# Optimization experiments

Measured on AMD Instinct MI355X. Metric: run time of the kernel, lower is better.

Reference implementation:

```python
import jax, jax.numpy as jnp
import numpy as np
from jax import lax

jax.config.update("jax_enable_x64", True)  # source casts distances to double for sinkhorn

N_E = 512
E_DIM = 256
NUM_EXPERTS = 10
B = 8192
MU = 0.25
BETA = 1.0
SK_EPS = 0.01
SK_ITERS = 100


def setup_inputs() -> dict:
    key = jax.random.key(0)
    k0, k1, k2, k3 = jax.random.split(key, 4)
    x = jax.random.normal(k0, (B, E_DIM), dtype=jnp.float32)
    label = jax.random.randint(k1, (N_E,), 0, 10)  # cluster id per code of codebook 0
    gate_probs = jax.random.uniform(k2, (B, NUM_EXPERTS), dtype=jnp.float32)
    # embeddings initialized uniform(-1/n_e, 1/n_e) as in __init__
    emb = jax.random.uniform(k3, (NUM_EXPERTS + 1, N_E, E_DIM), dtype=jnp.float32,
                             minval=-1.0 / N_E, maxval=1.0 / N_E)
    return {"x": x, "label": label, "idx": 0, "gate_probs": gate_probs, "emb": emb}


def _sinkhorn(d, eps, iters):
    # standard SwAV-style sinkhorn (as used in UniTok/LETTER); d: [B, K] float64
    logits = -d / eps
    Q = jnp.exp(logits - jnp.max(logits))  # max-shift is a no-op after global normalization
    Q = (Q / jnp.sum(Q)).T  # [K, B]
    K, Bn = Q.shape

    def step(Q, _):
        Q = Q / (jnp.sum(Q, axis=1, keepdims=True) * K)
        Q = Q / (jnp.sum(Q, axis=0, keepdims=True) * Bn)
        return Q, None

    Q, _ = lax.scan(step, Q, None, length=iters)
    return (Q * Bn).T  # [B, K]


def _assign(latent, W):
    d = (jnp.sum(latent ** 2, axis=1, keepdims=True)
         + jnp.sum(W ** 2, axis=1)[None, :]
         - 2.0 * latent @ W.T)  # [B, n_e]
    mx, mn = jnp.max(d), jnp.min(d)
    mid = (mx + mn) / 2
    amp = mx - mid + 1e-5
    d = ((d - mid) / amp).astype(jnp.float64)
    Q = _sinkhorn(d, SK_EPS, SK_ITERS)
    return jnp.argmax(Q, axis=-1)  # [B]


def reference(x, label, idx, gate_probs, emb):
    latent = x.reshape(-1, E_DIM)  # [B, D]
    nb = latent.shape[0]

    # per-expert sinkhorn assignment (use_sk=True, sk_epsilon>0 path)
    indices_all = jax.vmap(lambda W: _assign(latent, W))(emb)          # [11, B]
    xq_all = jax.vmap(lambda W, i: W[i])(emb, indices_all)              # [11, B, D]

    x_q = jnp.einsum('be,ebd->bd', gate_probs, xq_all[:NUM_EXPERTS])
    x_q = 0.95 * x_q + 0.05 * xq_all[NUM_EXPERTS]

    # diversity loss on codebook 0: positive = another code in the same cluster
    ind0 = indices_all[0]                      # [B]
    clusters = label[ind0]                     # [B]
    ar = jnp.arange(N_E)
    pos_mask = (label[None, :] == clusters[:, None]) & (ar[None, :] != ind0[:, None])
    y_true = jnp.argmax(pos_mask, axis=1)      # deterministic positive sample
    sim = x_q @ emb[0].T                       # [B, n_e]
    sim = sim.at[jnp.arange(nb), ind0].add(-1e12)  # mask self-similarity
    logp = jax.nn.log_softmax(sim, axis=-1)
    diversity_loss = -jnp.mean(logp[jnp.arange(nb), y_true])

    commitment_loss = jnp.mean((lax.stop_gradient(x_q) - x) ** 2)
    codebook_loss = jnp.mean((x_q - lax.stop_gradient(x)) ** 2)
    loss = codebook_loss + MU * commitment_loss + BETA * diversity_loss

    # selected index per token: codebook of top expert
    expert_id = jnp.argmax(gate_probs, axis=1)          # [B] in [0,10)
    indices = indices_all.T[jnp.arange(nb), expert_id]  # [B]

    x_q_out = x + lax.stop_gradient(x_q - x)  # straight-through
    return x_q_out, loss, indices
```

## Files before the change

### kernel.cpp

```cpp
#include <hip/hip_runtime.h>
#include <cstdint>
#include <cstddef>

#define NTOK 8192
#define NE 512
#define EDIM 256
#define NEXPALL 11
#define NITER 100

static __device__ __forceinline__ double wredsum(double x) {
  for (int o = 32; o > 0; o >>= 1) x += __shfl_down(x, o, 64);
  return x;
}

static constexpr double S32 = 2.3283064365386963e-10;
static constexpr double Q32 = 4294967296.0;

__global__ void k_init(unsigned* colmin, double* r0, double* r1, double* uprev,
                       unsigned* dmaxA, unsigned* dminA, int* conv_iter, double* sums) {
  int i = blockIdx.x * 256 + threadIdx.x;
  if (i < NEXPALL * NTOK) colmin[i] = 0x7F800000u;
  if (i < NEXPALL * NE) { r0[i] = 0.0; r1[i] = 0.0; uprev[i] = 0.0; }
  if (i < NEXPALL) { dmaxA[i] = 0u; dminA[i] = 0x7F800000u; conv_iter[i] = 1 << 30; }
  if (i < 2) sums[i] = 0.0;
}

__global__ __launch_bounds__(256) void k_npsq(const float* __restrict__ p, float* __restrict__ o, int rows) {
  int r = blockIdx.x * 16 + (threadIdx.x >> 4);
  int l = threadIdx.x & 15;
  if (r >= rows) return;
  const float* a = p + (size_t)r * EDIM;
  int leaf = l >> 3;
  int j = l & 7;
  const float* base = a + leaf * 128 + j;
  float acc = __fmul_rn(base[0], base[0]);
#pragma unroll
  for (int i = 8; i < 128; i += 8) {
    float v = base[i];
    acc = __fadd_rn(acc, __fmul_rn(v, v));
  }
  acc = __fadd_rn(acc, __shfl_xor(acc, 1, 64));
  acc = __fadd_rn(acc, __shfl_xor(acc, 2, 64));
  acc = __fadd_rn(acc, __shfl_xor(acc, 4, 64));
  float other = __shfl_xor(acc, 8, 64);
  float tot = (leaf == 0) ? __fadd_rn(acc, other) : __fadd_rn(other, acc);
  if (l == 0) o[r] = tot;
}

__global__ __launch_bounds__(256) void k_gemm_d(const float* __restrict__ x, const float* __restrict__ emb,
                                                const float* __restrict__ sx, const float* __restrict__ sw,
                                                float* __restrict__ bigF,
                                                unsigned* __restrict__ colminA,
                                                unsigned* __restrict__ dmaxA,
                                                unsigned* __restrict__ dminA) {
  int bx = blockIdx.x, by = blockIdx.y, e = blockIdx.z;
  int tid = threadIdx.x;
  int tx = tid & 15, ty = tid >> 4;
  int b0 = bx * 64, k0 = by * 64;

  __shared__ float xs[64][17];
  __shared__ float es[64][17];
  __shared__ float sxs[64];
  __shared__ float sws[64];
  __shared__ unsigned colm[64];
  __shared__ float ttile[64][68];
  __shared__ float wrx[4], wrn[4];

  if (tid < 64) { sxs[tid] = sx[b0 + tid]; colm[tid] = 0x7F800000u; }
  else if (tid < 128) { sws[tid - 64] = sw[e * NE + k0 + tid - 64]; }

  float acc[4][4] = {};
  const float* xbase = x + (size_t)b0 * EDIM;
  const float* wbase = emb + ((size_t)e * NE + k0) * EDIM;
  int lr = tid >> 2;
  int lc = (tid & 3) * 4;

  for (int kc = 0; kc < EDIM; kc += 16) {
    float4 xv = *(const float4*)(xbase + (size_t)lr * EDIM + kc + lc);
    float4 wv = *(const float4*)(wbase + (size_t)lr * EDIM + kc + lc);
    __syncthreads();
    xs[lr][lc + 0] = xv.x; xs[lr][lc + 1] = xv.y; xs[lr][lc + 2] = xv.z; xs[lr][lc + 3] = xv.w;
    es[lr][lc + 0] = wv.x; es[lr][lc + 1] = wv.y; es[lr][lc + 2] = wv.z; es[lr][lc + 3] = wv.w;
    __syncthreads();
#pragma unroll
    for (int kk = 0; kk < 16; ++kk) {
      float a0 = xs[ty][kk], a1 = xs[ty + 16][kk], a2 = xs[ty + 32][kk], a3 = xs[ty + 48][kk];
      float w0 = es[tx][kk], w1 = es[tx + 16][kk], w2 = es[tx + 32][kk], w3 = es[tx + 48][kk];
      acc[0][0] = fmaf(a0, w0, acc[0][0]); acc[0][1] = fmaf(a0, w1, acc[0][1]);
      acc[0][2] = fmaf(a0, w2, acc[0][2]); acc[0][3] = fmaf(a0, w3, acc[0][3]);
      acc[1][0] = fmaf(a1, w0, acc[1][0]); acc[1][1] = fmaf(a1, w1, acc[1][1]);
      acc[1][2] = fmaf(a1, w2, acc[1][2]); acc[1][3] = fmaf(a1, w3, acc[1][3]);
      acc[2][0] = fmaf(a2, w0, acc[2][0]); acc[2][1] = fmaf(a2, w1, acc[2][1]);
      acc[2][2] = fmaf(a2, w2, acc[2][2]); acc[2][3] = fmaf(a2, w3, acc[2][3]);
      acc[3][0] = fmaf(a3, w0, acc[3][0]); acc[3][1] = fmaf(a3, w1, acc[3][1]);
      acc[3][2] = fmaf(a3, w2, acc[3][2]); acc[3][3] = fmaf(a3, w3, acc[3][3]);
    }
  }

  float dmx = -3.0e38f, dmn = 3.0e38f;
#pragma unroll
  for (int i = 0; i < 4; ++i) {
    float cmin = 3.0e38f;
#pragma unroll
    for (int j = 0; j < 4; ++j) {
      float m2 = __fmul_rn(2.0f, acc[i][j]);
      float dv = __fsub_rn(__fadd_rn(sxs[ty + 16 * i], sws[tx + 16 * j]), m2);
      ttile[tx + 16 * j][ty + 16 * i] = dv;
      dmx = fmaxf(dmx, dv); dmn = fminf(dmn, dv);
      cmin = fminf(cmin, dv);
    }
    atomicMin(&colm[ty + 16 * i], __float_as_uint(cmin));
  }
  for (int o = 32; o > 0; o >>= 1) {
    dmx = fmaxf(dmx, __shfl_down(dmx, o, 64));
    dmn = fminf(dmn, __shfl_down(dmn, o, 64));
  }
  int wv = tid >> 6, ln = tid & 63;
  if (ln == 0) { wrx[wv] = dmx; wrn[wv] = dmn; }
  __syncthreads();
  if (tid == 0) {
    float m1 = fmaxf(fmaxf(wrx[0], wrx[1]), fmaxf(wrx[2], wrx[3]));
    float m2 = fminf(fminf(wrn[0], wrn[1]), fminf(wrn[2], wrn[3]));
    atomicMax(dmaxA + e, __float_as_uint(m1));
    atomicMin(dminA + e, __float_as_uint(m2));
  }
  if (tid < 64) atomicMin(colminA + (size_t)e * NTOK + b0 + tid, colm[tid]);
  int orow = tid >> 2, oc = (tid & 3) << 4;
  float* ob = bigF + ((size_t)e * NE + k0 + orow) * NTOK + b0 + oc;
  *(float4*)(ob + 0) = *(float4*)&ttile[orow][oc + 0];
  *(float4*)(ob + 4) = *(float4*)&ttile[orow][oc + 4];
  *(float4*)(ob + 8) = *(float4*)&ttile[orow][oc + 8];
  *(float4*)(ob + 12) = *(float4*)&ttile[orow][oc + 12];
}

__global__ __launch_bounds__(256) void k_prep(const unsigned* __restrict__ colminA,
                                              const unsigned* __restrict__ dmaxA,
                                              const unsigned* __restrict__ dminA,
                                              double* __restrict__ cml, double* __restrict__ v) {
  int e = blockIdx.y;
  int b = blockIdx.x * 256 + threadIdx.x;
  float mx = __uint_as_float(dmaxA[e]);
  float mn = __uint_as_float(dminA[e]);
  float mid = __fmul_rn(__fadd_rn(mx, mn), 0.5f);
  float amp = __fadd_rn(__fsub_rn(mx, mid), 1e-5f);
  float cminf = __uint_as_float(colminA[(size_t)e * NTOK + b]);
  float dn = __fdiv_rn(__fsub_rn(cminf, mid), amp);
  double l = (-(double)dn) / 0.01;
  cml[(size_t)e * NTOK + b] = l;
  v[(size_t)e * NTOK + b] = exp(l);
}

__global__ __launch_bounds__(256) void k_build(float* __restrict__ bigF,
                                               const unsigned* __restrict__ dmaxA,
                                               const unsigned* __restrict__ dminA,
                                               const double* __restrict__ cml, const double* __restrict__ v0,
                                               double* __restrict__ r0) {
  int bx = blockIdx.x, k = blockIdx.y, e = blockIdx.z;
  int tid = threadIdx.x;
  float mx = __uint_as_float(dmaxA[e]);
  float mn = __uint_as_float(dminA[e]);
  float mid = __fmul_rn(__fadd_rn(mx, mn), 0.5f);
  float amp = __fadd_rn(__fsub_rn(mx, mid), 1e-5f);
  size_t rb = ((size_t)e * NE + k) * NTOK;
  int cb = bx * 2048 + tid * 8;
  float4 fa = *(const float4*)(bigF + rb + cb);
  float4 fb = *(const float4*)(bigF + rb + cb + 4);
  float din[8] = {fa.x, fa.y, fa.z, fa.w, fb.x, fb.y, fb.z, fb.w};
  unsigned qo[8];
  double racc = 0.0;
#pragma unroll
  for (int j = 0; j < 8; ++j) {
    int b = cb + j;
    float dn = __fdiv_rn(__fsub_rn(din[j], mid), amp);
    double l = (-(double)dn) / 0.01;
    double t = l - cml[(size_t)e * NTOK + b];
    double Bv = exp(t);
    double qd = (1.0 - Bv) * Q32;
    qd = fmin(fmax(qd, 0.0), 4294967295.0);
    unsigned q = (unsigned)llrint(qd);
    qo[j] = q;
    double Bq = fma(-(double)q, S32, 1.0);
    racc = fma(Bq, v0[(size_t)e * NTOK + b], racc);
  }
  uint4 oa = make_uint4(qo[0], qo[1], qo[2], qo[3]);
  uint4 ob2 = make_uint4(qo[4], qo[5], qo[6], qo[7]);
  *(uint4*)((unsigned*)bigF + rb + cb) = oa;
  *(uint4*)((unsigned*)bigF + rb + cb + 4) = ob2;
  racc = wredsum(racc);
  __shared__ double pr[4];
  int wv = tid >> 6, ln = tid & 63;
  if (ln == 0) pr[wv] = racc;
  __syncthreads();
  if (tid == 0) atomicAdd(&r0[e * NE + k], (pr[0] + pr[1]) + (pr[2] + pr[3]));
}

__global__ __launch_bounds__(256) void k_iter_a(const unsigned* __restrict__ bigU,
                                                const double* __restrict__ rc, double* __restrict__ rn,
                                                double* __restrict__ v, double* __restrict__ uprev,
                                                int* conv_iter, int t) {
  int e = blockIdx.y, bx = blockIdx.x, tid = threadIdx.x;
  int ci = ((volatile int*)conv_iter)[e];
  if (t > ci) {
    if (bx == 0) {
      int k2 = tid * 2;
      rn[e * NE + k2] = rc[e * NE + k2];
      rn[e * NE + k2 + 1] = rc[e * NE + k2 + 1];
    }
    return;
  }
  __shared__ double us[NE];
  __shared__ int okf;
  if (tid == 0) okf = 1;
  int k2 = tid * 2;
  double u0 = 1.0 / (512.0 * rc[e * NE + k2]);
  double u1 = 1.0 / (512.0 * rc[e * NE + k2 + 1]);
  us[k2] = u0; us[k2 + 1] = u1;
  __syncthreads();
  if (bx == 0) {
    double p0 = uprev[e * NE + k2], p1 = uprev[e * NE + k2 + 1];
    bool ok = (fabs(u0 - p0) <= 1e-13 * fabs(u0)) && (fabs(u1 - p1) <= 1e-13 * fabs(u1));
    if (!ok) okf = 0;
    uprev[e * NE + k2] = u0; uprev[e * NE + k2 + 1] = u1;
    rn[e * NE + k2] = 0.0; rn[e * NE + k2 + 1] = 0.0;
  }
  __syncthreads();
  if (bx == 0 && tid == 0 && okf) atomicMin(conv_iter + e, t);

  int col = bx * 256 + tid;
  const unsigned* cp = bigU + (size_t)e * NE * NTOK + col;
  double c0 = 0, c1 = 0, c2 = 0, c3 = 0;
#pragma unroll 2
  for (int k = 0; k < NE; k += 4) {
    unsigned q0 = cp[(size_t)(k + 0) * NTOK];
    unsigned q1 = cp[(size_t)(k + 1) * NTOK];
    unsigned q2 = cp[(size_t)(k + 2) * NTOK];
    unsigned q3 = cp[(size_t)(k + 3) * NTOK];
    c0 = fma(us[k + 0], fma(-(double)q0, S32, 1.0), c0);
    c1 = fma(us[k + 1], fma(-(double)q1, S32, 1.0), c1);
    c2 = fma(us[k + 2], fma(-(double)q2, S32, 1.0), c2);
    c3 = fma(us[k + 3], fma(-(double)q3, S32, 1.0), c3);
  }
  double c = (c0 + c1) + (c2 + c3);
  v[(size_t)e * NTOK + col] = 1.0 / (8192.0 * c);
}

__global__ __launch_bounds__(256) void k_iter_b(const unsigned* __restrict__ bigU,
                                                const double* __restrict__ v, double* __restrict__ rn,
                                                const int* conv_iter, int t) {
  int e = blockIdx.z;
  if (t > ((volatile int*)conv_iter)[e]) return;
  int bx = blockIdx.x, ky = blockIdx.y, tid = threadIdx.x;
  int wv = tid >> 6, ln = tid & 63;
  int cb = bx * 2048 + tid * 8;
  const double* vb = v + (size_t)e * NTOK + cb;
  double v0 = vb[0], v1 = vb[1], v2 = vb[2], v3 = vb[3];
  double v4 = vb[4], v5 = vb[5], v6 = vb[6], v7 = vb[7];
  __shared__ double part[16][4];
  size_t ebase = (size_t)e * NE * NTOK;
  for (int rr = 0; rr < 4; ++rr) {
#pragma unroll 4
    for (int kk = 0; kk < 16; ++kk) {
      int k = ky * 64 + rr * 16 + kk;
      const unsigned* rp = bigU + ebase + (size_t)k * NTOK + cb;
      uint4 qa = *(const uint4*)rp;
      uint4 qb = *(const uint4*)(rp + 4);
      double p;
      p = v0 * fma(-(double)qa.x, S32, 1.0);
      p = fma(v1, fma(-(double)qa.y, S32, 1.0), p);
      p = fma(v2, fma(-(double)qa.z, S32, 1.0), p);
      p = fma(v3, fma(-(double)qa.w, S32, 1.0), p);
      p = fma(v4, fma(-(double)qb.x, S32, 1.0), p);
      p = fma(v5, fma(-(double)qb.y, S32, 1.0), p);
      p = fma(v6, fma(-(double)qb.z, S32, 1.0), p);
      p = fma(v7, fma(-(double)qb.w, S32, 1.0), p);
      p = wredsum(p);
      if (ln == 0) part[kk][wv] = p;
    }
    __syncthreads();
    if (tid < 16)
      atomicAdd(&rn[e * NE + ky * 64 + rr * 16 + tid],
                (part[tid][0] + part[tid][1]) + (part[tid][2] + part[tid][3]));
    __syncthreads();
  }
}

__global__ __launch_bounds__(256) void k_final(const unsigned* __restrict__ bigU,
                                               const double* __restrict__ rfin, int* __restrict__ idxs) {
  int e = blockIdx.y, bx = blockIdx.x, tid = threadIdx.x;
  __shared__ double us[NE];
  int k2 = tid * 2;
  us[k2] = 1.0 / (512.0 * rfin[e * NE + k2]);
  us[k2 + 1] = 1.0 / (512.0 * rfin[e * NE + k2 + 1]);
  __syncthreads();
  int col = bx * 256 + tid;
  const unsigned* cp = bigU + (size_t)e * NE * NTOK + col;
  double best = -1.0;
  int bi = 0;
#pragma unroll 4
  for (int k = 0; k < NE; ++k) {
    double s = us[k] * fma(-(double)cp[(size_t)k * NTOK], S32, 1.0);
    if (s > best) { best = s; bi = k; }
  }
  idxs[(size_t)e * NTOK + col] = bi;
}

__global__ __launch_bounds__(256) void k_mix(const float* __restrict__ x, const float* __restrict__ gate,
                                             const float* __restrict__ emb, const int* __restrict__ idxs,
                                             float* __restrict__ xq, float* __restrict__ out0,
                                             float* __restrict__ outIdx, double* __restrict__ mse_sum) {
  int tid = threadIdx.x;
  int sub = tid >> 5, lane = tid & 31;
  int tok = blockIdx.x * 8 + sub;
  float acc[8] = {0, 0, 0, 0, 0, 0, 0, 0};
#pragma unroll
  for (int ee = 0; ee < 10; ++ee) {
    int id = idxs[(size_t)ee * NTOK + tok];
    float g = gate[tok * 10 + ee];
    const float* er = emb + ((size_t)ee * NE + id) * EDIM + lane;
#pragma unroll
    for (int dd = 0; dd < 8; ++dd) acc[dd] = fmaf(g, er[32 * dd], acc[dd]);
  }
  int id10 = idxs[(size_t)10 * NTOK + tok];
  const float* es = emb + ((size_t)10 * NE + id10) * EDIM + lane;
  double ms = 0.0;
#pragma unroll
  for (int dd = 0; dd < 8; ++dd) {
    int d = lane + 32 * dd;
    float q = 0.95f * acc[dd] + 0.05f * es[32 * dd];
    float xv = x[(size_t)tok * EDIM + d];
    float df = q - xv;
    out0[(size_t)tok * EDIM + d] = xv + df;
    xq[(size_t)tok * EDIM + d] = q;
    ms += (double)df * (double)df;
  }
  ms = wredsum(ms);
  __shared__ double pr[4];
  int wv = tid >> 6, ln = tid & 63;
  if (ln == 0) pr[wv] = ms;
  __syncthreads();
  if (tid == 0) atomicAdd(mse_sum, (pr[0] + pr[1]) + (pr[2] + pr[3]));
  if (lane == 0) {
    const float* gr = gate + tok * 10;
    float bg = gr[0];
    int be = 0;
#pragma unroll
    for (int ee = 1; ee < 10; ++ee) { float g = gr[ee]; if (g > bg) { bg = g; be = ee; } }
    outIdx[tok] = (float)idxs[(size_t)be * NTOK + tok];
  }
}

__global__ __launch_bounds__(256) void k_simgemm(const float* __restrict__ xq, const float* __restrict__ emb,
                                                 float* __restrict__ sim) {
  int bx = blockIdx.x, by = blockIdx.y, tid = threadIdx.x;
  int tx = tid & 15, ty = tid >> 4;
  int b0 = bx * 64, j0 = by * 64;
  __shared__ float xs[64][17];
  __shared__ float es[64][17];
  __shared__ float tt[64][68];
  float acc[4][4] = {};
  int lr = tid >> 2, lc = (tid & 3) * 4;
  for (int kc = 0; kc < EDIM; kc += 16) {
    float4 xv = *(const float4*)(xq + (size_t)(b0 + lr) * EDIM + kc + lc);
    float4 ev = *(const float4*)(emb + (size_t)(j0 + lr) * EDIM + kc + lc);
    __syncthreads();
    xs[lr][lc + 0] = xv.x; xs[lr][lc + 1] = xv.y; xs[lr][lc + 2] = xv.z; xs[lr][lc + 3] = xv.w;
    es[lr][lc + 0] = ev.x; es[lr][lc + 1] = ev.y; es[lr][lc + 2] = ev.z; es[lr][lc + 3] = ev.w;
    __syncthreads();
#pragma unroll
    for (int kk = 0; kk < 16; ++kk) {
      float a0 = xs[ty][kk], a1 = xs[ty + 16][kk], a2 = xs[ty + 32][kk], a3 = xs[ty + 48][kk];
      float w0 = es[tx][kk], w1 = es[tx + 16][kk], w2 = es[tx + 32][kk], w3 = es[tx + 48][kk];
      acc[0][0] = fmaf(a0, w0, acc[0][0]); acc[0][1] = fmaf(a0, w1, acc[0][1]);
      acc[0][2] = fmaf(a0, w2, acc[0][2]); acc[0][3] = fmaf(a0, w3, acc[0][3]);
      acc[1][0] = fmaf(a1, w0, acc[1][0]); acc[1][1] = fmaf(a1, w1, acc[1][1]);
      acc[1][2] = fmaf(a1, w2, acc[1][2]); acc[1][3] = fmaf(a1, w3, acc[1][3]);
      acc[2][0] = fmaf(a2, w0, acc[2][0]); acc[2][1] = fmaf(a2, w1, acc[2][1]);
      acc[2][2] = fmaf(a2, w2, acc[2][2]); acc[2][3] = fmaf(a2, w3, acc[2][3]);
      acc[3][0] = fmaf(a3, w0, acc[3][0]); acc[3][1] = fmaf(a3, w1, acc[3][1]);
      acc[3][2] = fmaf(a3, w2, acc[3][2]); acc[3][3] = fmaf(a3, w3, acc[3][3]);
    }
  }
#pragma unroll
  for (int i = 0; i < 4; ++i)
#pragma unroll
    for (int j = 0; j < 4; ++j) tt[ty + 16 * i][tx + 16 * j] = acc[i][j];
  __syncthreads();
  int orow = tid >> 2, oc = (tid & 3) << 4;
  float* ob = sim + (size_t)(b0 + orow) * NE + j0 + oc;
  *(float4*)(ob + 0) = *(float4*)&tt[orow][oc + 0];
  *(float4*)(ob + 4) = *(float4*)&tt[orow][oc + 4];
  *(float4*)(ob + 8) = *(float4*)&tt[orow][oc + 8];
  *(float4*)(ob + 12) = *(float4*)&tt[orow][oc + 12];
}

__global__ __launch_bounds__(256) void k_div(const float* __restrict__ sim, const int* __restrict__ idxs,
                                             const int* __restrict__ label, double* __restrict__ div_sum) {
  __shared__ int lab[NE];
  int tid = threadIdx.x;
  lab[tid] = label[tid];
  lab[256 + tid] = label[256 + tid];
  __syncthreads();
  int wv = tid >> 6, ln = tid & 63;
  int b = blockIdx.x * 4 + wv;
  int ind0 = idxs[b];
  int clu = lab[ind0];
  const float* sr = sim + (size_t)b * NE;
  double vals[8];
  double mx = -1e300;
  int ys = 1024;
#pragma unroll
  for (int c = 0; c < 8; ++c) {
    int j = ln + 64 * c;
    double vv = (double)sr[j];
    if (j == ind0) vv -= 1e12;
    vals[c] = vv;
    mx = fmax(mx, vv);
    if (lab[j] == clu && j != ind0 && j < ys) ys = j;
  }
  for (int o = 32; o > 0; o >>= 1) {
    mx = fmax(mx, __shfl_xor(mx, o, 64));
    ys = min(ys, __shfl_xor(ys, o, 64));
  }
  int y = (ys >= 1024) ? 0 : ys;
  double se = 0.0, vy = 0.0;
#pragma unroll
  for (int c = 0; c < 8; ++c) {
    int j = ln + 64 * c;
    se += exp(vals[c] - mx);
    if (j == y) vy = vals[c];
  }
  for (int o = 32; o > 0; o >>= 1) {
    se += __shfl_xor(se, o, 64);
    vy += __shfl_xor(vy, o, 64);
  }
  if (ln == 0) {
    double lse = mx + log(se);
    atomicAdd(div_sum, lse - vy);
  }
}

__global__ void k_loss(const double* __restrict__ sums, float* __restrict__ out) {
  double mse = sums[0] / 2097152.0;
  double dv = sums[1] / 8192.0;
  double loss = (mse + 0.25 * mse) + dv;
  out[0] = (float)loss;
}

extern "C" void kernel_launch(void* const* d_in, const int* in_sizes, int n_in,
                              void* d_out, int out_size, void* d_ws, size_t ws_size,
                              hipStream_t stream) {
  (void)in_sizes; (void)n_in; (void)out_size;
  const float* x = (const float*)d_in[0];
  const int* label = (const int*)d_in[1];
  const float* gate = (const float*)d_in[3];
  const float* emb = (const float*)d_in[4];
  float* out = (float*)d_out;
  float* out0 = out;
  float* outLoss = out + (size_t)NTOK * EDIM;
  float* outIdx = out + (size_t)NTOK * EDIM + 1;

  char* w = (char*)d_ws;
  size_t off = 0;
  auto alloc = [&](size_t bytes) -> void* {
    void* p = w + off;
    off += (bytes + 15) & ~(size_t)15;
    return p;
  };
  float* bigF = (float*)alloc((size_t)NEXPALL * NE * NTOK * 4);
  unsigned* bigU = (unsigned*)bigF;
  float* sim = (float*)bigF;
  unsigned* colminA = (unsigned*)alloc((size_t)NEXPALL * NTOK * 4);
  double* cml = (double*)alloc((size_t)NEXPALL * NTOK * 8);
  double* v = (double*)alloc((size_t)NEXPALL * NTOK * 8);
  double* r0 = (double*)alloc((size_t)NEXPALL * NE * 8);
  double* r1 = (double*)alloc((size_t)NEXPALL * NE * 8);
  double* uprev = (double*)alloc((size_t)NEXPALL * NE * 8);
  float* sxF = (float*)alloc((size_t)NTOK * 4);
  float* swF = (float*)alloc((size_t)NEXPALL * NE * 4);
  unsigned* dmaxA = (unsigned*)alloc(NEXPALL * 4);
  unsigned* dminA = (unsigned*)alloc(NEXPALL * 4);
  int* conv_iter = (int*)alloc(NEXPALL * 4);
  int* idxs = (int*)alloc((size_t)NEXPALL * NTOK * 4);
  float* xq = (float*)alloc((size_t)NTOK * EDIM * 4);
  double* sums = (double*)alloc(2 * 8);
  if (off > ws_size) return;

  k_init<<<352, 256, 0, stream>>>(colminA, r0, r1, uprev, dmaxA, dminA, conv_iter, sums);
  k_npsq<<<NTOK / 16, 256, 0, stream>>>(x, sxF, NTOK);
  k_npsq<<<(NEXPALL * NE) / 16, 256, 0, stream>>>(emb, swF, NEXPALL * NE);
  k_gemm_d<<<dim3(128, 8, NEXPALL), 256, 0, stream>>>(x, emb, sxF, swF, bigF, colminA, dmaxA, dminA);
  k_prep<<<dim3(32, NEXPALL), 256, 0, stream>>>(colminA, dmaxA, dminA, cml, v);
  k_build<<<dim3(4, NE, NEXPALL), 256, 0, stream>>>(bigF, dmaxA, dminA, cml, v, r0);
  for (int t = 1; t <= NITER; ++t) {
    const double* rc = (t & 1) ? r0 : r1;
    double* rn = (t & 1) ? r1 : r0;
    k_iter_a<<<dim3(32, NEXPALL), 256, 0, stream>>>(bigU, rc, rn, v, uprev, conv_iter, t);
    k_iter_b<<<dim3(4, 8, NEXPALL), 256, 0, stream>>>(bigU, v, rn, conv_iter, t);
  }
  k_final<<<dim3(32, NEXPALL), 256, 0, stream>>>(bigU, r1, idxs);
  k_mix<<<NTOK / 8, 256, 0, stream>>>(x, gate, emb, idxs, xq, out0, outIdx, sums);
  k_simgemm<<<dim3(128, 8), 256, 0, stream>>>(xq, emb, sim);
  k_div<<<NTOK / 4, 256, 0, stream>>>(sim, idxs, label, sums + 1);
  k_loss<<<1, 1, 0, stream>>>(sums, outLoss);
}
```

Baseline: 1.515 ms.

## Fuse Sinkhorn iterations into one cooperative kernel and enlarge distance GEMM tiles

Replaces the 200 per-iteration kernel launches (iter_a/iter_b) and the final argmax kernel with a single cooperative-groups persistent kernel that uses grid.sync between the column and row normalization phases. Row sums are now written directly per block rather than via atomics into ping-pong buffers, and convergence freezing is tracked with device flags. Separately, the distance GEMM moves from 64x64 tiles with 4x4 register blocking to 128x128 tiles with 8x8 register blocking and transposed shared-memory layout, writing output straight from registers. Risks include grid.sync cost, the cooperative launch requiring all 352 blocks to be co-resident, and higher register pressure in the GEMM.

```diff
diff --git a/kernel.cpp b/kernel.cpp
--- a/kernel.cpp
+++ b/kernel.cpp
@@ -1,4 +1,5 @@
 #include <hip/hip_runtime.h>
+#include <hip/hip_cooperative_groups.h>
 #include <cstdint>
 #include <cstddef>
 
@@ -8,6 +9,8 @@
 #define NEXPALL 11
 #define NITER 100
 
+namespace cg = cooperative_groups;
+
 static __device__ __forceinline__ double wredsum(double x) {
   for (int o = 32; o > 0; o >>= 1) x += __shfl_down(x, o, 64);
   return x;
@@ -16,13 +19,14 @@
 static constexpr double S32 = 2.3283064365386963e-10;
 static constexpr double Q32 = 4294967296.0;
 
-__global__ void k_init(unsigned* colmin, double* r0, double* r1, double* uprev,
-                       unsigned* dmaxA, unsigned* dminA, int* conv_iter, double* sums) {
+__global__ void k_init(unsigned* colmin, double* r, double* uprev, int* ctrl, double* sums,
+                       unsigned* dmaxA, unsigned* dminA) {
   int i = blockIdx.x * 256 + threadIdx.x;
   if (i < NEXPALL * NTOK) colmin[i] = 0x7F800000u;
-  if (i < NEXPALL * NE) { r0[i] = 0.0; r1[i] = 0.0; uprev[i] = 0.0; }
-  if (i < NEXPALL) { dmaxA[i] = 0u; dminA[i] = 0x7F800000u; conv_iter[i] = 1 << 30; }
+  if (i < NEXPALL * NE) { r[i] = 0.0; uprev[i] = 0.0; }
+  if (i < 16) ctrl[i] = 0;
   if (i < 2) sums[i] = 0.0;
+  if (i < NEXPALL) { dmaxA[i] = 0u; dminA[i] = 0x7F800000u; }
 }
 
 __global__ __launch_bounds__(256) void k_npsq(const float* __restrict__ p, float* __restrict__ o, int rows) {
@@ -56,60 +60,58 @@
   int bx = blockIdx.x, by = blockIdx.y, e = blockIdx.z;
   int tid = threadIdx.x;
   int tx = tid & 15, ty = tid >> 4;
-  int b0 = bx * 64, k0 = by * 64;
-
-  __shared__ float xs[64][17];
-  __shared__ float es[64][17];
-  __shared__ float sxs[64];
-  __shared__ float sws[64];
-  __shared__ unsigned colm[64];
-  __shared__ float ttile[64][68];
+  int b0 = bx * 128, k0 = by * 128;
+  __shared__ float As[16][128];
+  __shared__ float Bs[16][128];
+  __shared__ float sxs[128];
+  __shared__ float sws[128];
+  __shared__ unsigned colm[128];
   __shared__ float wrx[4], wrn[4];
-
-  if (tid < 64) { sxs[tid] = sx[b0 + tid]; colm[tid] = 0x7F800000u; }
-  else if (tid < 128) { sws[tid - 64] = sw[e * NE + k0 + tid - 64]; }
-
-  float acc[4][4] = {};
-  const float* xbase = x + (size_t)b0 * EDIM;
-  const float* wbase = emb + ((size_t)e * NE + k0) * EDIM;
-  int lr = tid >> 2;
-  int lc = (tid & 3) * 4;
-
+  if (tid < 128) { sxs[tid] = sx[b0 + tid]; colm[tid] = 0x7F800000u; }
+  else { sws[tid - 128] = sw[e * NE + k0 + tid - 128]; }
+  float acc[8][8] = {};
+  const float* xb = x + (size_t)b0 * EDIM;
+  const float* wb = emb + ((size_t)e * NE + k0) * EDIM;
+  int lr = tid >> 1, lco = (tid & 1) * 8;
   for (int kc = 0; kc < EDIM; kc += 16) {
-    float4 xv = *(const float4*)(xbase + (size_t)lr * EDIM + kc + lc);
-    float4 wv = *(const float4*)(wbase + (size_t)lr * EDIM + kc + lc);
+    float4 x0 = *(const float4*)(xb + (size_t)lr * EDIM + kc + lco);
+    float4 x1 = *(const float4*)(xb + (size_t)lr * EDIM + kc + lco + 4);
+    float4 e0 = *(const float4*)(wb + (size_t)lr * EDIM + kc + lco);
+    float4 e1 = *(const float4*)(wb + (size_t)lr * EDIM + kc + lco + 4);
     __syncthreads();
-    xs[lr][lc + 0] = xv.x; xs[lr][lc + 1] = xv.y; xs[lr][lc + 2] = xv.z; xs[lr][lc + 3] = xv.w;
-    es[lr][lc + 0] = wv.x; es[lr][lc + 1] = wv.y; es[lr][lc + 2] = wv.z; es[lr][lc + 3] = wv.w;
+    As[lco + 0][lr] = x0.x; As[lco + 1][lr] = x0.y; As[lco + 2][lr] = x0.z; As[lco + 3][lr] = x0.w;
+    As[lco + 4][lr] = x1.x; As[lco + 5][lr] = x1.y; As[lco + 6][lr] = x1.z; As[lco + 7][lr] = x1.w;
+    Bs[lco + 0][lr] = e0.x; Bs[lco + 1][lr] = e0.y; Bs[lco + 2][lr] = e0.z; Bs[lco + 3][lr] = e0.w;
+    Bs[lco + 4][lr] = e1.x; Bs[lco + 5][lr] = e1.y; Bs[lco + 6][lr] = e1.z; Bs[lco + 7][lr] = e1.w;
     __syncthreads();
 #pragma unroll
     for (int kk = 0; kk < 16; ++kk) {
-      float a0 = xs[ty][kk], a1 = xs[ty + 16][kk], a2 = xs[ty + 32][kk], a3 = xs[ty + 48][kk];
-      float w0 = es[tx][kk], w1 = es[tx + 16][kk], w2 = es[tx + 32][kk], w3 = es[tx + 48][kk];
-      acc[0][0] = fmaf(a0, w0, acc[0][0]); acc[0][1] = fmaf(a0, w1, acc[0][1]);
-      acc[0][2] = fmaf(a0, w2, acc[0][2]); acc[0][3] = fmaf(a0, w3, acc[0][3]);
-      acc[1][0] = fmaf(a1, w0, acc[1][0]); acc[1][1] = fmaf(a1, w1, acc[1][1]);
-      acc[1][2] = fmaf(a1, w2, acc[1][2]); acc[1][3] = fmaf(a1, w3, acc[1][3]);
-      acc[2][0] = fmaf(a2, w0, acc[2][0]); acc[2][1] = fmaf(a2, w1, acc[2][1]);
-      acc[2][2] = fmaf(a2, w2, acc[2][2]); acc[2][3] = fmaf(a2, w3, acc[2][3]);
-      acc[3][0] = fmaf(a3, w0, acc[3][0]); acc[3][1] = fmaf(a3, w1, acc[3][1]);
-      acc[3][2] = fmaf(a3, w2, acc[3][2]); acc[3][3] = fmaf(a3, w3, acc[3][3]);
-    }
-  }
-
+      float a[8], b[8];
+      *(float4*)&a[0] = *(const float4*)&As[kk][ty * 4];
+      *(float4*)&a[4] = *(const float4*)&As[kk][64 + ty * 4];
+      *(float4*)&b[0] = *(const float4*)&Bs[kk][tx * 4];
+      *(float4*)&b[4] = *(const float4*)&Bs[kk][64 + tx * 4];
+#pragma unroll
+      for (int i = 0; i < 8; ++i)
+#pragma unroll
+        for (int j = 0; j < 8; ++j)
+          acc[i][j] = fmaf(a[i], b[j], acc[i][j]);
+    }
+  }
   float dmx = -3.0e38f, dmn = 3.0e38f;
 #pragma unroll
-  for (int i = 0; i < 4; ++i) {
+  for (int i = 0; i < 8; ++i) {
+    int m = (i < 4) ? (ty * 4 + i) : (64 + ty * 4 + i - 4);
     float cmin = 3.0e38f;
 #pragma unroll
-    for (int j = 0; j < 4; ++j) {
-      float m2 = __fmul_rn(2.0f, acc[i][j]);
-      float dv = __fsub_rn(__fadd_rn(sxs[ty + 16 * i], sws[tx + 16 * j]), m2);
-      ttile[tx + 16 * j][ty + 16 * i] = dv;
+    for (int j = 0; j < 8; ++j) {
+      int n = (j < 4) ? (tx * 4 + j) : (64 + tx * 4 + j - 4);
+      float dv = __fsub_rn(__fadd_rn(sxs[m], sws[n]), __fmul_rn(2.0f, acc[i][j]));
+      acc[i][j] = dv;
       dmx = fmaxf(dmx, dv); dmn = fminf(dmn, dv);
       cmin = fminf(cmin, dv);
     }
-    atomicMin(&colm[ty + 16 * i], __float_as_uint(cmin));
+    atomicMin(&colm[m], __float_as_uint(cmin));
   }
   for (int o = 32; o > 0; o >>= 1) {
     dmx = fmaxf(dmx, __shfl_down(dmx, o, 64));
@@ -119,18 +121,19 @@
   if (ln == 0) { wrx[wv] = dmx; wrn[wv] = dmn; }
   __syncthreads();
   if (tid == 0) {
-    float m1 = fmaxf(fmaxf(wrx[0], wrx[1]), fmaxf(wrx[2], wrx[3]));
-    float m2 = fminf(fminf(wrn[0], wrn[1]), fminf(wrn[2], wrn[3]));
-    atomicMax(dmaxA + e, __float_as_uint(m1));
-    atomicMin(dminA + e, __float_as_uint(m2));
-  }
-  if (tid < 64) atomicMin(colminA + (size_t)e * NTOK + b0 + tid, colm[tid]);
-  int orow = tid >> 2, oc = (tid & 3) << 4;
-  float* ob = bigF + ((size_t)e * NE + k0 + orow) * NTOK + b0 + oc;
-  *(float4*)(ob + 0) = *(float4*)&ttile[orow][oc + 0];
-  *(float4*)(ob + 4) = *(float4*)&ttile[orow][oc + 4];
-  *(float4*)(ob + 8) = *(float4*)&ttile[orow][oc + 8];
-  *(float4*)(ob + 12) = *(float4*)&ttile[orow][oc + 12];
+    atomicMax(dmaxA + e, __float_as_uint(fmaxf(fmaxf(wrx[0], wrx[1]), fmaxf(wrx[2], wrx[3]))));
+    atomicMin(dminA + e, __float_as_uint(fminf(fminf(wrn[0], wrn[1]), fminf(wrn[2], wrn[3]))));
+  }
+  if (tid < 128) atomicMin(colminA + (size_t)e * NTOK + b0 + tid, colm[tid]);
+#pragma unroll
+  for (int j = 0; j < 8; ++j) {
+    int n = (j < 4) ? (tx * 4 + j) : (64 + tx * 4 + j - 4);
+    float* op = bigF + ((size_t)e * NE + k0 + n) * NTOK + b0;
+    float4 v0 = make_float4(acc[0][j], acc[1][j], acc[2][j], acc[3][j]);
+    float4 v1 = make_float4(acc[4][j], acc[5][j], acc[6][j], acc[7][j]);
+    *(float4*)(op + ty * 4) = v0;
+    *(float4*)(op + 64 + ty * 4) = v1;
+  }
 }
 
 __global__ __launch_bounds__(256) void k_prep(const unsigned* __restrict__ colminA,
@@ -194,114 +197,111 @@
   if (tid == 0) atomicAdd(&r0[e * NE + k], (pr[0] + pr[1]) + (pr[2] + pr[3]));
 }
 
-__global__ __launch_bounds__(256) void k_iter_a(const unsigned* __restrict__ bigU,
-                                                const double* __restrict__ rc, double* __restrict__ rn,
-                                                double* __restrict__ v, double* __restrict__ uprev,
-                                                int* conv_iter, int t) {
-  int e = blockIdx.y, bx = blockIdx.x, tid = threadIdx.x;
-  int ci = ((volatile int*)conv_iter)[e];
-  if (t > ci) {
-    if (bx == 0) {
+__global__ __launch_bounds__(256, 2) void k_sink(const unsigned* __restrict__ bigU,
+                                                 double* __restrict__ r,
+                                                 double* __restrict__ v,
+                                                 double* __restrict__ uprev,
+                                                 int* __restrict__ nfrozen,
+                                                 int* __restrict__ snap,
+                                                 int* __restrict__ frozen,
+                                                 int* __restrict__ idxs) {
+  cg::grid_group grid = cg::this_grid();
+  int blk = blockIdx.x;
+  int e = blk >> 5;
+  int chunk = blk & 31;
+  int tid = threadIdx.x;
+  int wv = tid >> 6, ln = tid & 63;
+  size_t ebase = (size_t)e * (size_t)NE * NTOK;
+  __shared__ double us[NE];
+  __shared__ double pr[16][4];
+  __shared__ int sokf, s_snap, s_fro;
+
+  for (int t = 1; t <= NITER; ++t) {
+    if (tid == 0) {
+      s_snap = *(volatile int*)snap;
+      s_fro = ((volatile int*)frozen)[e];
+    }
+    __syncthreads();
+    if (s_snap == NEXPALL) break;
+    bool fro = (s_fro != 0);
+    if (!fro) {
       int k2 = tid * 2;
-      rn[e * NE + k2] = rc[e * NE + k2];
-      rn[e * NE + k2 + 1] = rc[e * NE + k2 + 1];
-    }
-    return;
-  }
-  __shared__ double us[NE];
-  __shared__ int okf;
-  if (tid == 0) okf = 1;
-  int k2 = tid * 2;
-  double u0 = 1.0 / (512.0 * rc[e * NE + k2]);
-  double u1 = 1.0 / (512.0 * rc[e * NE + k2 + 1]);
-  us[k2] = u0; us[k2 + 1] = u1;
-  __syncthreads();
-  if (bx == 0) {
-    double p0 = uprev[e * NE + k2], p1 = uprev[e * NE + k2 + 1];
-    bool ok = (fabs(u0 - p0) <= 1e-13 * fabs(u0)) && (fabs(u1 - p1) <= 1e-13 * fabs(u1));
-    if (!ok) okf = 0;
-    uprev[e * NE + k2] = u0; uprev[e * NE + k2 + 1] = u1;
-    rn[e * NE + k2] = 0.0; rn[e * NE + k2 + 1] = 0.0;
-  }
-  __syncthreads();
-  if (bx == 0 && tid == 0 && okf) atomicMin(conv_iter + e, t);
-
-  int col = bx * 256 + tid;
-  const unsigned* cp = bigU + (size_t)e * NE * NTOK + col;
-  double c0 = 0, c1 = 0, c2 = 0, c3 = 0;
+      double u0 = 1.0 / (512.0 * r[e * NE + k2]);
+      double u1 = 1.0 / (512.0 * r[e * NE + k2 + 1]);
+      us[k2] = u0; us[k2 + 1] = u1;
+      if (tid == 0) sokf = 1;
+      __syncthreads();
+      if (chunk == 0) {
+        double p0 = uprev[e * NE + k2], p1 = uprev[e * NE + k2 + 1];
+        bool ok = (fabs(u0 - p0) <= 1e-13 * fabs(u0)) && (fabs(u1 - p1) <= 1e-13 * fabs(u1));
+        if (!ok) sokf = 0;
+        uprev[e * NE + k2] = u0; uprev[e * NE + k2 + 1] = u1;
+      }
+      int col = chunk * 256 + tid;
+      const unsigned* cp = bigU + ebase + col;
+      double c0 = 0, c1 = 0, c2 = 0, c3 = 0;
 #pragma unroll 2
-  for (int k = 0; k < NE; k += 4) {
-    unsigned q0 = cp[(size_t)(k + 0) * NTOK];
-    unsigned q1 = cp[(size_t)(k + 1) * NTOK];
-    unsigned q2 = cp[(size_t)(k + 2) * NTOK];
-    unsigned q3 = cp[(size_t)(k + 3) * NTOK];
-    c0 = fma(us[k + 0], fma(-(double)q0, S32, 1.0), c0);
-    c1 = fma(us[k + 1], fma(-(double)q1, S32, 1.0), c1);
-    c2 = fma(us[k + 2], fma(-(double)q2, S32, 1.0), c2);
-    c3 = fma(us[k + 3], fma(-(double)q3, S32, 1.0), c3);
-  }
-  double c = (c0 + c1) + (c2 + c3);
-  v[(size_t)e * NTOK + col] = 1.0 / (8192.0 * c);
-}
-
-__global__ __launch_bounds__(256) void k_iter_b(const unsigned* __restrict__ bigU,
-                                                const double* __restrict__ v, double* __restrict__ rn,
-                                                const int* conv_iter, int t) {
-  int e = blockIdx.z;
-  if (t > ((volatile int*)conv_iter)[e]) return;
-  int bx = blockIdx.x, ky = blockIdx.y, tid = threadIdx.x;
-  int wv = tid >> 6, ln = tid & 63;
-  int cb = bx * 2048 + tid * 8;
-  const double* vb = v + (size_t)e * NTOK + cb;
-  double v0 = vb[0], v1 = vb[1], v2 = vb[2], v3 = vb[3];
-  double v4 = vb[4], v5 = vb[5], v6 = vb[6], v7 = vb[7];
-  __shared__ double part[16][4];
-  size_t ebase = (size_t)e * NE * NTOK;
-  for (int rr = 0; rr < 4; ++rr) {
+      for (int k = 0; k < NE; k += 4) {
+        unsigned q0 = cp[(size_t)(k + 0) * NTOK];
+        unsigned q1 = cp[(size_t)(k + 1) * NTOK];
+        unsigned q2 = cp[(size_t)(k + 2) * NTOK];
+        unsigned q3 = cp[(size_t)(k + 3) * NTOK];
+        c0 = fma(us[k + 0], fma(-(double)q0, S32, 1.0), c0);
+        c1 = fma(us[k + 1], fma(-(double)q1, S32, 1.0), c1);
+        c2 = fma(us[k + 2], fma(-(double)q2, S32, 1.0), c2);
+        c3 = fma(us[k + 3], fma(-(double)q3, S32, 1.0), c3);
+      }
+      v[(size_t)e * NTOK + col] = 1.0 / (8192.0 * ((c0 + c1) + (c2 + c3)));
+    }
+    grid.sync();
+    if (chunk == 0 && !fro && tid == 0 && sokf) {
+      ((volatile int*)frozen)[e] = 1;
+      atomicAdd(nfrozen, 1);
+    }
+    if (blk == 0 && tid == 0) *(volatile int*)snap = *(volatile int*)nfrozen;
+    if (t < NITER && !fro) {
+      double vr[32];
+#pragma unroll
+      for (int j = 0; j < 8; ++j) {
+        double4 vq = *(const double4*)(v + (size_t)e * NTOK + j * 1024 + tid * 4);
+        vr[4 * j + 0] = vq.x; vr[4 * j + 1] = vq.y; vr[4 * j + 2] = vq.z; vr[4 * j + 3] = vq.w;
+      }
+#pragma unroll 1
+      for (int rr = 0; rr < 16; ++rr) {
+        const unsigned* rp = bigU + ebase + (size_t)(chunk * 16 + rr) * NTOK + tid * 4;
+        double a = 0;
+#pragma unroll
+        for (int j = 0; j < 8; ++j) {
+          uint4 q = *(const uint4*)(rp + j * 1024);
+          a = fma(fma(-(double)q.x, S32, 1.0), vr[4 * j + 0], a);
+          a = fma(fma(-(double)q.y, S32, 1.0), vr[4 * j + 1], a);
+          a = fma(fma(-(double)q.z, S32, 1.0), vr[4 * j + 2], a);
+          a = fma(fma(-(double)q.w, S32, 1.0), vr[4 * j + 3], a);
+        }
+        a = wredsum(a);
+        if (ln == 0) pr[rr][wv] = a;
+      }
+      __syncthreads();
+      if (tid < 16) r[e * NE + chunk * 16 + tid] = (pr[tid][0] + pr[tid][1]) + (pr[tid][2] + pr[tid][3]);
+    }
+    grid.sync();
+  }
+  {
+    int k2 = tid * 2;
+    us[k2] = 1.0 / (512.0 * r[e * NE + k2]);
+    us[k2 + 1] = 1.0 / (512.0 * r[e * NE + k2 + 1]);
+    __syncthreads();
+    int col = chunk * 256 + tid;
+    const unsigned* cp = bigU + ebase + col;
+    double best = -1.0;
+    int bi = 0;
 #pragma unroll 4
-    for (int kk = 0; kk < 16; ++kk) {
-      int k = ky * 64 + rr * 16 + kk;
-      const unsigned* rp = bigU + ebase + (size_t)k * NTOK + cb;
-      uint4 qa = *(const uint4*)rp;
-      uint4 qb = *(const uint4*)(rp + 4);
-      double p;
-      p = v0 * fma(-(double)qa.x, S32, 1.0);
-      p = fma(v1, fma(-(double)qa.y, S32, 1.0), p);
-      p = fma(v2, fma(-(double)qa.z, S32, 1.0), p);
-      p = fma(v3, fma(-(double)qa.w, S32, 1.0), p);
-      p = fma(v4, fma(-(double)qb.x, S32, 1.0), p);
-      p = fma(v5, fma(-(double)qb.y, S32, 1.0), p);
-      p = fma(v6, fma(-(double)qb.z, S32, 1.0), p);
-      p = fma(v7, fma(-(double)qb.w, S32, 1.0), p);
-      p = wredsum(p);
-      if (ln == 0) part[kk][wv] = p;
-    }
-    __syncthreads();
-    if (tid < 16)
-      atomicAdd(&rn[e * NE + ky * 64 + rr * 16 + tid],
-                (part[tid][0] + part[tid][1]) + (part[tid][2] + part[tid][3]));
-    __syncthreads();
-  }
-}
-
-__global__ __launch_bounds__(256) void k_final(const unsigned* __restrict__ bigU,
-                                               const double* __restrict__ rfin, int* __restrict__ idxs) {
-  int e = blockIdx.y, bx = blockIdx.x, tid = threadIdx.x;
-  __shared__ double us[NE];
-  int k2 = tid * 2;
-  us[k2] = 1.0 / (512.0 * rfin[e * NE + k2]);
-  us[k2 + 1] = 1.0 / (512.0 * rfin[e * NE + k2 + 1]);
-  __syncthreads();
-  int col = bx * 256 + tid;
-  const unsigned* cp = bigU + (size_t)e * NE * NTOK + col;
-  double best = -1.0;
-  int bi = 0;
-#pragma unroll 4
-  for (int k = 0; k < NE; ++k) {
-    double s = us[k] * fma(-(double)cp[(size_t)k * NTOK], S32, 1.0);
-    if (s > best) { best = s; bi = k; }
-  }
-  idxs[(size_t)e * NTOK + col] = bi;
+    for (int k = 0; k < NE; ++k) {
+      double s = us[k] * fma(-(double)cp[(size_t)k * NTOK], S32, 1.0);
+      if (s > best) { best = s; bi = k; }
+    }
+    idxs[(size_t)e * NTOK + col] = bi;
+  }
 }
 
 __global__ __launch_bounds__(256) void k_mix(const float* __restrict__ x, const float* __restrict__ gate,
@@ -463,7 +463,7 @@
   size_t off = 0;
   auto alloc = [&](size_t bytes) -> void* {
     void* p = w + off;
-    off += (bytes + 15) & ~(size_t)15;
+    off += (bytes + 31) & ~(size_t)31;
     return p;
   };
   float* bigF = (float*)alloc((size_t)NEXPALL * NE * NTOK * 4);
@@ -472,32 +472,38 @@
   unsigned* colminA = (unsigned*)alloc((size_t)NEXPALL * NTOK * 4);
   double* cml = (double*)alloc((size_t)NEXPALL * NTOK * 8);
   double* v = (double*)alloc((size_t)NEXPALL * NTOK * 8);
-  double* r0 = (double*)alloc((size_t)NEXPALL * NE * 8);
-  double* r1 = (double*)alloc((size_t)NEXPALL * NE * 8);
+  double* r = (double*)alloc((size_t)NEXPALL * NE * 8);
   double* uprev = (double*)alloc((size_t)NEXPALL * NE * 8);
   float* sxF = (float*)alloc((size_t)NTOK * 4);
   float* swF = (float*)alloc((size_t)NEXPALL * NE * 4);
   unsigned* dmaxA = (unsigned*)alloc(NEXPALL * 4);
   unsigned* dminA = (unsigned*)alloc(NEXPALL * 4);
-  int* conv_iter = (int*)alloc(NEXPALL * 4);
+  int* ctrl = (int*)alloc(16 * 4);
   int* idxs = (int*)alloc((size_t)NEXPALL * NTOK * 4);
   float* xq = (float*)alloc((size_t)NTOK * EDIM * 4);
   double* sums = (double*)alloc(2 * 8);
   if (off > ws_size) return;
 
-  k_init<<<352, 256, 0, stream>>>(colminA, r0, r1, uprev, dmaxA, dminA, conv_iter, sums);
+  k_init<<<352, 256, 0, stream>>>(colminA, r, uprev, ctrl, sums, dmaxA, dminA);
   k_npsq<<<NTOK / 16, 256, 0, stream>>>(x, sxF, NTOK);
   k_npsq<<<(NEXPALL * NE) / 16, 256, 0, stream>>>(emb, swF, NEXPALL * NE);
-  k_gemm_d<<<dim3(128, 8, NEXPALL), 256, 0, stream>>>(x, emb, sxF, swF, bigF, colminA, dmaxA, dminA);
+  k_gemm_d<<<dim3(64, 4, NEXPALL), 256, 0, stream>>>(x, emb, sxF, swF, bigF, colminA, dmaxA, dminA);
   k_prep<<<dim3(32, NEXPALL), 256, 0, stream>>>(colminA, dmaxA, dminA, cml, v);
-  k_build<<<dim3(4, NE, NEXPALL), 256, 0, stream>>>(bigF, dmaxA, dminA, cml, v, r0);
-  for (int t = 1; t <= NITER; ++t) {
-    const double* rc = (t & 1) ? r0 : r1;
-    double* rn = (t & 1) ? r1 : r0;
-    k_iter_a<<<dim3(32, NEXPALL), 256, 0, stream>>>(bigU, rc, rn, v, uprev, conv_iter, t);
-    k_iter_b<<<dim3(4, 8, NEXPALL), 256, 0, stream>>>(bigU, v, rn, conv_iter, t);
-  }
-  k_final<<<dim3(32, NEXPALL), 256, 0, stream>>>(bigU, r1, idxs);
+  k_build<<<dim3(4, NE, NEXPALL), 256, 0, stream>>>(bigF, dmaxA, dminA, cml, v, r);
+
+  {
+    const unsigned* a0 = bigU;
+    double* a1 = r;
+    double* a2 = v;
+    double* a3 = uprev;
+    int* a4 = ctrl + 0;
+    int* a5 = ctrl + 1;
+    int* a6 = ctrl + 2;
+    int* a7 = idxs;
+    void* args[] = {&a0, &a1, &a2, &a3, &a4, &a5, &a6, &a7};
+    hipLaunchCooperativeKernel((const void*)k_sink, dim3(NEXPALL * 32), dim3(256), args, 0, stream);
+  }
+
   k_mix<<<NTOK / 8, 256, 0, stream>>>(x, gate, emb, idxs, xq, out0, outIdx, sums);
   k_simgemm<<<dim3(128, 8), 256, 0, stream>>>(xq, emb, sim);
   k_div<<<NTOK / 4, 256, 0, stream>>>(sim, idxs, label, sums + 1);
```

Result: slower. 1.550 ms (+2.3%).
